# Optimization experiments

Hardware: AMD Instinct MI355X
Metric: run time of the kernel (lower is better)

## Reference

```python
import jax, jax.numpy as jnp
import numpy as np

N_HEADS = 32
N_KV_HEADS = 8
HEAD_DIM = 64
D_MODEL = 2048
SLIDING_WINDOW = 512
ROPE_THETA = 10000.0
PAST_LENGTH = 0
EPS = 1e-6


def setup_inputs() -> dict:
    key = jax.random.key(0)
    k1, k2, k3 = jax.random.split(key, 3)
    B, S = 1, 2048
    q_size = N_HEADS * HEAD_DIM
    kv_size = N_KV_HEADS * HEAD_DIM
    return {
        "x": jax.random.normal(k1, (B, S, D_MODEL), dtype=jnp.float32),
        "w_qkv": jax.random.normal(k2, (q_size + 2 * kv_size, D_MODEL), dtype=jnp.float32) * (D_MODEL ** -0.5),
        "w_out": jax.random.normal(k3, (D_MODEL, q_size), dtype=jnp.float32) * (q_size ** -0.5),
        "q_norm_w": jnp.ones((HEAD_DIM,), dtype=jnp.float32),
        "k_norm_w": jnp.ones((HEAD_DIM,), dtype=jnp.float32),
    }


def _rms_norm(x, w):
    xf = x.astype(jnp.float32)
    rms = jax.lax.rsqrt(jnp.mean(xf * xf, axis=-1, keepdims=True) + EPS)
    return (xf * rms).astype(x.dtype) * w


def _rope(q, k, past_length):
    # q: [b, h, s, d], k: [b, kv, s, d]
    s, d = q.shape[2], q.shape[3]
    inv_freq = 1.0 / (ROPE_THETA ** (jnp.arange(0, d, 2, dtype=jnp.float32) / d))
    pos = jnp.arange(s, dtype=jnp.float32) + past_length
    ang = pos[:, None] * inv_freq[None, :]            # [s, d/2]
    emb = jnp.concatenate([ang, ang], axis=-1)        # [s, d]
    cos, sin = jnp.cos(emb), jnp.sin(emb)

    def rot_half(x):
        x1, x2 = jnp.split(x, 2, axis=-1)
        return jnp.concatenate([-x2, x1], axis=-1)

    q = q * cos + rot_half(q) * sin
    k = k * cos + rot_half(k) * sin
    return q, k


def _sliding_mask(seq_len, total_len, past_length):
    q_idx = jnp.arange(seq_len)[:, None]
    k_idx = jnp.arange(total_len)[None, :]
    causal = (q_idx + past_length) >= k_idx
    window = (q_idx + past_length - k_idx) < SLIDING_WINDOW
    keep = causal & window
    return jnp.where(keep, 0.0, -jnp.inf).astype(jnp.float32)[None, None]


def reference(x, w_qkv, w_out, q_norm_w, k_norm_w):
    b, s, _ = x.shape
    n_rep = N_HEADS // N_KV_HEADS
    q_size = N_HEADS * HEAD_DIM
    kv_size = N_KV_HEADS * HEAD_DIM

    qkv = jnp.einsum('bsd,od->bso', x, w_qkv)
    q, k, v = jnp.split(qkv, [q_size, q_size + kv_size], axis=-1)
    q = q.reshape(b, s, N_HEADS, HEAD_DIM).transpose(0, 2, 1, 3)
    k = k.reshape(b, s, N_KV_HEADS, HEAD_DIM).transpose(0, 2, 1, 3)
    v = v.reshape(b, s, N_KV_HEADS, HEAD_DIM).transpose(0, 2, 1, 3)

    q = _rms_norm(q, q_norm_w)
    k = _rms_norm(k, k_norm_w)
    q, k = _rope(q, k, PAST_LENGTH)

    k_rep = jnp.repeat(k, n_rep, axis=1)  # [b, H, s, d]
    v_rep = jnp.repeat(v, n_rep, axis=1)

    scale = HEAD_DIM ** -0.5
    scores = jnp.einsum('bhqd,bhkd->bhqk', q, k_rep) * scale
    scores = scores + _sliding_mask(s, s, PAST_LENGTH)
    probs = jax.nn.softmax(scores, axis=-1)
    attn = jnp.einsum('bhqk,bhkd->bhqd', probs, v_rep)

    attn = attn.transpose(0, 2, 1, 3).reshape(b, s, q_size)
    return jnp.einsum('bso,do->bsd', attn, w_out)
```

## Files before the change

kernel.cpp:

```cpp
#include <hip/hip_runtime.h>

typedef unsigned short u16;
typedef unsigned int u32;
typedef __bf16 bf16x8 __attribute__((ext_vector_type(8)));
typedef float f32x4 __attribute__((ext_vector_type(4)));
typedef float f32x16 __attribute__((ext_vector_type(16)));
typedef u16 u16x8 __attribute__((ext_vector_type(8)));
typedef u32 u32x2 __attribute__((ext_vector_type(2)));
typedef u32 u32x4 __attribute__((ext_vector_type(4)));

#define MFMA16(a, b, c) __builtin_amdgcn_mfma_f32_16x16x32_bf16((a), (b), (c), 0, 0, 0)
#define MFMA32(a, b, c) __builtin_amdgcn_mfma_f32_32x32x16_bf16((a), (b), (c), 0, 0, 0)

__device__ __forceinline__ u16 f2bf(float f) {
    unsigned int u = __float_as_uint(f);
    u = (u + 0x7FFF + ((u >> 16) & 1)) >> 16;
    return (u16)u;
}

__device__ __forceinline__ u32 cvtpk(float a, float b) {
    u32 d;
    asm("v_cvt_pk_bf16_f32 %0, %1, %2" : "=v"(d) : "v"(a), "v"(b));
    return d;
}

__device__ __forceinline__ void gld_lds16(const u16* g, u16* l) {
    __builtin_amdgcn_global_load_lds(
        (const __attribute__((address_space(1))) unsigned int*)g,
        (__attribute__((address_space(3))) unsigned int*)l, 16, 0, 0);
}

__global__ __launch_bounds__(256) void cvt_bf16(const float* __restrict__ in,
                                                u16* __restrict__ out, int n4) {
    int idx = blockIdx.x * blockDim.x + threadIdx.x;
    int stride = gridDim.x * blockDim.x;
    for (int i = idx; i < n4; i += stride) {
        float4 v = reinterpret_cast<const float4*>(in)[i];
        ushort4 o;
        o.x = f2bf(v.x); o.y = f2bf(v.y); o.z = f2bf(v.z); o.w = f2bf(v.w);
        reinterpret_cast<ushort4*>(out)[i] = o;
    }
}

__global__ __launch_bounds__(256) void reduce_add(const float4* __restrict__ a,
                                                  const float4* __restrict__ b,
                                                  float4* __restrict__ o, int n4) {
    int idx = blockIdx.x * blockDim.x + threadIdx.x;
    int stride = gridDim.x * blockDim.x;
    for (int i = idx; i < n4; i += stride) {
        float4 va = a[i], vb = b[i];
        float4 vo = {va.x + vb.x, va.y + vb.y, va.z + vb.z, va.w + vb.w};
        o[i] = vo;
    }
}

template <int SPLITK>
__global__ __launch_bounds__(256) void gemm_bt(const u16* __restrict__ A,
                                               const u16* __restrict__ B,
                                               float* __restrict__ C,
                                               int M, int N, int K) {
    __shared__ __align__(16) u16 As[2][128 * 32];
    __shared__ __align__(16) u16 Bs[2][128 * 32];

    int nbn = N >> 7;
    int bid = blockIdx.x;
    int nwg = (M >> 7) * nbn;
    int cpx = nwg >> 3;
    int wg = (bid & 7) * cpx + (bid >> 3);
    int tm = wg / nbn, tn = wg % nbn;
    int m0 = tm << 7, n0 = tn << 7;

    int Ks = K / SPLITK;
    int kbase = blockIdx.y * Ks;
    float* Cs = C + (size_t)blockIdx.y * ((size_t)M * N);

    int t = threadIdx.x;
    int w = t >> 6, l = t & 63, lrow = l & 15, lhi = l >> 4;
    int wr = w >> 1, wc = w & 1;

    int e0 = t * 8;
    int row0 = e0 >> 5, col0 = e0 & 31;

    const u16* Ag = A + (size_t)m0 * K + kbase;
    const u16* Bg = B + (size_t)n0 * K + kbase;

    auto stage = [&](int sbuf, int kt) {
        int k0 = kt << 5;
        gld_lds16(Ag + (size_t)row0 * K + k0 + col0, &As[sbuf][e0]);
        gld_lds16(Ag + (size_t)(row0 + 64) * K + k0 + col0, &As[sbuf][e0 + 2048]);
        gld_lds16(Bg + (size_t)row0 * K + k0 + col0, &Bs[sbuf][e0]);
        gld_lds16(Bg + (size_t)(row0 + 64) * K + k0 + col0, &Bs[sbuf][e0 + 2048]);
    };

    f32x4 acc[4][4] = {};
    int NT = Ks >> 5;
    stage(0, 0);
    __syncthreads();
    int buf = 0;
    for (int kt = 0; kt < NT; ++kt) {
        if (kt + 1 < NT) stage(buf ^ 1, kt + 1);
        bf16x8 af[4], bfr[4];
#pragma unroll
        for (int i = 0; i < 4; ++i) {
            af[i]  = *(const bf16x8*)&As[buf][(wr * 64 + i * 16 + lrow) * 32 + lhi * 8];
            bfr[i] = *(const bf16x8*)&Bs[buf][(wc * 64 + i * 16 + lrow) * 32 + lhi * 8];
        }
#pragma unroll
        for (int i = 0; i < 4; ++i)
#pragma unroll
            for (int j = 0; j < 4; ++j)
                acc[i][j] = MFMA16(af[i], bfr[j], acc[i][j]);
        __syncthreads();
        buf ^= 1;
    }
#pragma unroll
    for (int i = 0; i < 4; ++i) {
#pragma unroll
        for (int j = 0; j < 4; ++j) {
            int crow = m0 + wr * 64 + i * 16 + lhi * 4;
            int ccol = n0 + wc * 64 + j * 16 + lrow;
            float* cp = Cs + (size_t)crow * N + ccol;
#pragma unroll
            for (int r2 = 0; r2 < 4; ++r2) cp[(size_t)r2 * N] = acc[i][j][r2];
        }
    }
}

__global__ __launch_bounds__(256) void qkv_post(const float* __restrict__ qkv0,
                                                const float* __restrict__ qkv1,
                                                const float* __restrict__ qw,
                                                const float* __restrict__ kw,
                                                u16* __restrict__ qb,
                                                u16* __restrict__ kb,
                                                u16* __restrict__ vb) {
    const float C = 0.18033688011112042f;
    int s = blockIdx.x;
    int t = threadIdx.x, w = t >> 6, lane = t & 63;
    const float* row0 = qkv0 + (size_t)s * 3072;
    const float* row1 = qkv1 + (size_t)s * 3072;
    int d2 = lane & 31;
    float inv = exp2f(-(float)d2 * (13.287712379549449f / 32.0f));
    float ang = (float)s * inv;
    float cs = cosf(ang), sn = sinf(ang);
    for (int h = w; h < 48; h += 4) {
        float v = row0[h * 64 + lane] + row1[h * 64 + lane];
        if (h < 40) {
            float ss = v * v;
#pragma unroll
            for (int m = 32; m; m >>= 1) ss += __shfl_xor(ss, m);
            float rms = rsqrtf(ss * (1.0f / 64.0f) + 1e-6f);
            float wgt = (h < 32) ? qw[lane] : kw[lane];
            v = v * rms * wgt;
            float part = __shfl_xor(v, 32);
            float rot = (lane < 32) ? -part : part;
            v = v * cs + rot * sn;
            if (h < 32)
                qb[((size_t)h * 2048 + s) * 64 + lane] = f2bf(v * C);
            else
                kb[((size_t)(h - 32) * 2048 + s) * 64 + lane] = f2bf(v);
        } else {
            vb[((size_t)(h - 40) * 2048 + s) * 64 + lane] = f2bf(v);
        }
    }
}

__global__ __launch_bounds__(256) void transpose_v(const u16* __restrict__ vb,
                                                   u16* __restrict__ vt) {
    int kv = blockIdx.y;
    int s0 = blockIdx.x * 256;
    __shared__ __align__(16) u16 tile[64][256];
    int t = threadIdx.x;
    int sl = t >> 3;
    int d0 = (t & 7) * 8;
#pragma unroll
    for (int j = 0; j < 8; ++j) {
        int s = sl + j * 32;
        u16x8 v = *(const u16x8*)(vb + ((size_t)kv * 2048 + s0 + s) * 64 + d0);
#pragma unroll
        for (int e = 0; e < 8; ++e) tile[d0 + e][s] = v[e];
    }
    __syncthreads();
    int d = t >> 2;
    int so = (t & 3) * 64;
#pragma unroll
    for (int j = 0; j < 8; ++j) {
        int s_local = so + j * 8;
        *(u16x8*)(vt + ((size_t)kv * 64 + d) * 2048 + s0 + s_local) =
            *(const u16x8*)&tile[d][s_local];
    }
}

__global__ __launch_bounds__(256) void attn_fa4(const u16* __restrict__ qb,
                                                const u16* __restrict__ kb,
                                                const u16* __restrict__ vt,
                                                u16* __restrict__ ab) {
    int h = blockIdx.y, kv = h >> 2;
    int t = threadIdx.x, w = t >> 6, l = t & 63;
    int lq = l & 31, hi = l >> 5;
    int qlo = blockIdx.x * 32;
    __shared__ float Olds[4][64][32];
    __shared__ float llds[4][32];

    const u16* qrow = qb + ((size_t)h * 2048 + qlo + lq) * 64 + hi * 8;
    bf16x8 qf[4];
#pragma unroll
    for (int dk = 0; dk < 4; ++dk) qf[dk] = *(const bf16x8*)(qrow + dk * 16);

    f32x16 oa = {}, ob = {};
    float lsum = 0.f;

    int kstart = qlo - 511; if (kstart < 0) kstart = 0;
    int kt0 = kstart >> 5, kt1 = qlo >> 5;
    const u16* kb_h = kb + (size_t)kv * 2048 * 64;
    const u16* vt_h = vt + (size_t)kv * 64 * 2048;

    for (int kt = kt0 + w; kt <= kt1; kt += 4) {
        int k0 = kt << 5;
        const u16* krow = kb_h + (size_t)(k0 + lq) * 64 + hi * 8;
        bf16x8 kf0 = *(const bf16x8*)(krow);
        bf16x8 kf1 = *(const bf16x8*)(krow + 16);
        bf16x8 kf2 = *(const bf16x8*)(krow + 32);
        bf16x8 kf3 = *(const bf16x8*)(krow + 48);
        const u16* vrow = vt_h + (size_t)lq * 2048 + k0 + hi * 8;
        bf16x8 va0 = *(const bf16x8*)(vrow);
        bf16x8 va1 = *(const bf16x8*)(vrow + 16);
        bf16x8 vb0 = *(const bf16x8*)(vrow + 32 * 2048);
        bf16x8 vb1 = *(const bf16x8*)(vrow + 32 * 2048 + 16);

        f32x16 s = {};
        s = MFMA32(kf0, qf[0], s);
        s = MFMA32(kf1, qf[1], s);
        s = MFMA32(kf2, qf[2], s);
        s = MFMA32(kf3, qf[3], s);

        bool edge = (k0 + 31 > qlo) || (qlo + 31 - k0 >= 512);
        if (edge) {
            int q = qlo + lq;
#pragma unroll
            for (int r = 0; r < 16; ++r) {
                int k = k0 + (r & 3) + 8 * (r >> 2) + 4 * hi;
                if (!((unsigned)(q - k) < 512u)) s[r] = -1e30f;
            }
        }
        float p[16];
#pragma unroll
        for (int r = 0; r < 16; ++r) {
            p[r] = exp2f(s[r]);
            lsum += p[r];
        }

        u32 pk0 = cvtpk(p[0], p[1]),   pk1 = cvtpk(p[2], p[3]);
        u32 pk2 = cvtpk(p[4], p[5]),   pk3 = cvtpk(p[6], p[7]);
        u32 pk4 = cvtpk(p[8], p[9]),   pk5 = cvtpk(p[10], p[11]);
        u32 pk6 = cvtpk(p[12], p[13]), pk7 = cvtpk(p[14], p[15]);
        u32x2 r02 = __builtin_amdgcn_permlane32_swap(pk0, pk2, false, false);
        u32x2 r13 = __builtin_amdgcn_permlane32_swap(pk1, pk3, false, false);
        u32x2 r46 = __builtin_amdgcn_permlane32_swap(pk4, pk6, false, false);
        u32x2 r57 = __builtin_amdgcn_permlane32_swap(pk5, pk7, false, false);
        bf16x8 b0, b1;
        {
            u32* bp = (u32*)&b0;
            bp[0] = r02[0]; bp[1] = r13[0]; bp[2] = r02[1]; bp[3] = r13[1];
            u32* bq = (u32*)&b1;
            bq[0] = r46[0]; bq[1] = r57[0]; bq[2] = r46[1]; bq[3] = r57[1];
        }
        oa = MFMA32(va0, b0, oa);
        oa = MFMA32(va1, b1, oa);
        ob = MFMA32(vb0, b0, ob);
        ob = MFMA32(vb1, b1, ob);
    }

    lsum += __shfl_xor(lsum, 32);
#pragma unroll
    for (int r = 0; r < 16; ++r) {
        int d = (r & 3) + 8 * (r >> 2) + 4 * hi;
        Olds[w][d][lq]      = oa[r];
        Olds[w][d + 32][lq] = ob[r];
    }
    if (hi == 0) llds[w][lq] = lsum;
    __syncthreads();

    int q = t & 31, dg = t >> 5;
    float lt = llds[0][q] + llds[1][q] + llds[2][q] + llds[3][q];
    float inv = 1.0f / lt;
    float v[8];
#pragma unroll
    for (int e = 0; e < 8; ++e) {
        int d = dg * 8 + e;
        v[e] = (Olds[0][d][q] + Olds[1][d][q] +
                Olds[2][d][q] + Olds[3][d][q]) * inv;
    }
    u32x4 pkt = { cvtpk(v[0], v[1]), cvtpk(v[2], v[3]),
                  cvtpk(v[4], v[5]), cvtpk(v[6], v[7]) };
    *(u32x4*)(ab + (size_t)(qlo + q) * 2048 + h * 64 + dg * 8) = pkt;
}

extern "C" void kernel_launch(void* const* d_in, const int* in_sizes, int n_in,
                              void* d_out, int out_size, void* d_ws, size_t ws_size,
                              hipStream_t stream) {
    const float* x     = (const float*)d_in[0];
    const float* w_qkv = (const float*)d_in[1];
    const float* w_out = (const float*)d_in[2];
    const float* qw    = (const float*)d_in[3];
    const float* kw    = (const float*)d_in[4];
    float* out = (float*)d_out;

    char* ws = (char*)d_ws;
    u16*   x_b    = (u16*)(ws);
    u16*   wB     = (u16*)(ws + 8388608);
    u16*   q_b    = (u16*)(ws);
    u16*   k_b    = (u16*)(ws + 8388608);
    u16*   v_b    = (u16*)(ws + 10485760);
    u16*   v_t    = (u16*)(ws + 12582912);
    float* P0     = (float*)(ws + 20971520);
    float* O0     = (float*)(ws + 20971520);
    float* O1     = (float*)(ws + 37748736);
    u16*   attn_b = (u16*)(ws + 54525952);

    cvt_bf16<<<2048, 256, 0, stream>>>(x, x_b, 2048 * 2048 / 4);
    cvt_bf16<<<2048, 256, 0, stream>>>(w_qkv, wB, 3072 * 2048 / 4);
    gemm_bt<2><<<dim3(384, 2), 256, 0, stream>>>(x_b, wB, P0, 2048, 3072, 2048);
    qkv_post<<<2048, 256, 0, stream>>>(P0, P0 + (size_t)2048 * 3072, qw, kw, q_b, k_b, v_b);
    transpose_v<<<dim3(8, 8), 256, 0, stream>>>(v_b, v_t);
    attn_fa4<<<dim3(64, 32), 256, 0, stream>>>(q_b, k_b, v_t, attn_b);
    cvt_bf16<<<2048, 256, 0, stream>>>(w_out, wB, 2048 * 2048 / 4);
    gemm_bt<2><<<dim3(256, 2), 256, 0, stream>>>(attn_b, wB, O0, 2048, 2048, 2048);
    reduce_add<<<1024, 256, 0, stream>>>((const float4*)O0, (const float4*)O1,
                                         (float4*)out, 2048 * 2048 / 4);
}
```

Measured before the change: 147.1 us.

## Use 8-wave GEMM tiles and software-prefetch K tiles in attention

The bf16 GEMM now launches 512 threads per block with a 2x4 wave grid. Each wave computes a 64x32 sub-tile, so staging needs one global-to-LDS load per thread per operand instead of two. This should raise occupancy and latency hiding at the cost of more B-fragment LDS reads per MFMA. The attention kernel double-buffers the K fragments in registers, loading the next tile's K while the current tile is computed, to overlap global-load latency with MFMA and softmax work; this costs extra registers.

```diff
diff --git a/kernel.cpp b/kernel.cpp
--- a/kernel.cpp
+++ b/kernel.cpp
@@ -55,7 +55,7 @@
 }
 
 template <int SPLITK>
-__global__ __launch_bounds__(256) void gemm_bt(const u16* __restrict__ A,
+__global__ __launch_bounds__(512) void gemm_bt(const u16* __restrict__ A,
                                                const u16* __restrict__ B,
                                                float* __restrict__ C,
                                                int M, int N, int K) {
@@ -76,7 +76,7 @@
 
     int t = threadIdx.x;
     int w = t >> 6, l = t & 63, lrow = l & 15, lhi = l >> 4;
-    int wr = w >> 1, wc = w & 1;
+    int wr = w >> 2, wc = w & 3;
 
     int e0 = t * 8;
     int row0 = e0 >> 5, col0 = e0 & 31;
@@ -87,28 +87,27 @@
     auto stage = [&](int sbuf, int kt) {
         int k0 = kt << 5;
         gld_lds16(Ag + (size_t)row0 * K + k0 + col0, &As[sbuf][e0]);
-        gld_lds16(Ag + (size_t)(row0 + 64) * K + k0 + col0, &As[sbuf][e0 + 2048]);
         gld_lds16(Bg + (size_t)row0 * K + k0 + col0, &Bs[sbuf][e0]);
-        gld_lds16(Bg + (size_t)(row0 + 64) * K + k0 + col0, &Bs[sbuf][e0 + 2048]);
     };
 
-    f32x4 acc[4][4] = {};
+    f32x4 acc[4][2] = {};
     int NT = Ks >> 5;
     stage(0, 0);
     __syncthreads();
     int buf = 0;
     for (int kt = 0; kt < NT; ++kt) {
         if (kt + 1 < NT) stage(buf ^ 1, kt + 1);
-        bf16x8 af[4], bfr[4];
-#pragma unroll
-        for (int i = 0; i < 4; ++i) {
-            af[i]  = *(const bf16x8*)&As[buf][(wr * 64 + i * 16 + lrow) * 32 + lhi * 8];
-            bfr[i] = *(const bf16x8*)&Bs[buf][(wc * 64 + i * 16 + lrow) * 32 + lhi * 8];
-        }
+        bf16x8 af[4], bfr[2];
 #pragma unroll
         for (int i = 0; i < 4; ++i)
-#pragma unroll
-            for (int j = 0; j < 4; ++j)
+            af[i] = *(const bf16x8*)&As[buf][(wr * 64 + i * 16 + lrow) * 32 + lhi * 8];
+#pragma unroll
+        for (int j = 0; j < 2; ++j)
+            bfr[j] = *(const bf16x8*)&Bs[buf][(wc * 32 + j * 16 + lrow) * 32 + lhi * 8];
+#pragma unroll
+        for (int i = 0; i < 4; ++i)
+#pragma unroll
+            for (int j = 0; j < 2; ++j)
                 acc[i][j] = MFMA16(af[i], bfr[j], acc[i][j]);
         __syncthreads();
         buf ^= 1;
@@ -116,9 +115,9 @@
 #pragma unroll
     for (int i = 0; i < 4; ++i) {
 #pragma unroll
-        for (int j = 0; j < 4; ++j) {
+        for (int j = 0; j < 2; ++j) {
             int crow = m0 + wr * 64 + i * 16 + lhi * 4;
-            int ccol = n0 + wc * 64 + j * 16 + lrow;
+            int ccol = n0 + wc * 32 + j * 16 + lrow;
             float* cp = Cs + (size_t)crow * N + ccol;
 #pragma unroll
             for (int r2 = 0; r2 < 4; ++r2) cp[(size_t)r2 * N] = acc[i][j][r2];
@@ -190,7 +189,7 @@
     }
 }
 
-__global__ __launch_bounds__(256) void attn_fa4(const u16* __restrict__ qb,
+__global__ __launch_bounds__(256) void attn_fa5(const u16* __restrict__ qb,
                                                 const u16* __restrict__ kb,
                                                 const u16* __restrict__ vt,
                                                 u16* __restrict__ ab) {
@@ -214,25 +213,22 @@
     const u16* kb_h = kb + (size_t)kv * 2048 * 64;
     const u16* vt_h = vt + (size_t)kv * 64 * 2048;
 
-    for (int kt = kt0 + w; kt <= kt1; kt += 4) {
-        int k0 = kt << 5;
-        const u16* krow = kb_h + (size_t)(k0 + lq) * 64 + hi * 8;
-        bf16x8 kf0 = *(const bf16x8*)(krow);
-        bf16x8 kf1 = *(const bf16x8*)(krow + 16);
-        bf16x8 kf2 = *(const bf16x8*)(krow + 32);
-        bf16x8 kf3 = *(const bf16x8*)(krow + 48);
-        const u16* vrow = vt_h + (size_t)lq * 2048 + k0 + hi * 8;
-        bf16x8 va0 = *(const bf16x8*)(vrow);
-        bf16x8 va1 = *(const bf16x8*)(vrow + 16);
-        bf16x8 vb0 = *(const bf16x8*)(vrow + 32 * 2048);
-        bf16x8 vb1 = *(const bf16x8*)(vrow + 32 * 2048 + 16);
-
+#define LOADK(k0_, f0, f1, f2, f3)                                          \
+    { const u16* kr_ = kb_h + (size_t)((k0_) + lq) * 64 + hi * 8;           \
+      f0 = *(const bf16x8*)(kr_);       f1 = *(const bf16x8*)(kr_ + 16);    \
+      f2 = *(const bf16x8*)(kr_ + 32);  f3 = *(const bf16x8*)(kr_ + 48); }
+#define LOADV(k0_, a0, a1, b0, b1)                                          \
+    { const u16* vr_ = vt_h + (size_t)lq * 2048 + (k0_) + hi * 8;           \
+      a0 = *(const bf16x8*)(vr_);              a1 = *(const bf16x8*)(vr_ + 16); \
+      b0 = *(const bf16x8*)(vr_ + 32 * 2048);  b1 = *(const bf16x8*)(vr_ + 32 * 2048 + 16); }
+
+    auto dotile = [&](int k0, bf16x8 kf0, bf16x8 kf1, bf16x8 kf2, bf16x8 kf3,
+                      bf16x8 va0, bf16x8 va1, bf16x8 vb0, bf16x8 vb1) {
         f32x16 s = {};
         s = MFMA32(kf0, qf[0], s);
         s = MFMA32(kf1, qf[1], s);
         s = MFMA32(kf2, qf[2], s);
         s = MFMA32(kf3, qf[3], s);
-
         bool edge = (k0 + 31 > qlo) || (qlo + 31 - k0 >= 512);
         if (edge) {
             int q = qlo + lq;
@@ -248,7 +244,6 @@
             p[r] = exp2f(s[r]);
             lsum += p[r];
         }
-
         u32 pk0 = cvtpk(p[0], p[1]),   pk1 = cvtpk(p[2], p[3]);
         u32 pk2 = cvtpk(p[4], p[5]),   pk3 = cvtpk(p[6], p[7]);
         u32 pk4 = cvtpk(p[8], p[9]),   pk5 = cvtpk(p[10], p[11]);
@@ -268,7 +263,25 @@
         oa = MFMA32(va1, b1, oa);
         ob = MFMA32(vb0, b0, ob);
         ob = MFMA32(vb1, b1, ob);
-    }
+    };
+
+    bf16x8 kA0, kA1, kA2, kA3, kB0, kB1, kB2, kB3;
+    bf16x8 va0, va1, vb0, vb1;
+    int kt = kt0 + w;
+    if (kt <= kt1) LOADK(kt << 5, kA0, kA1, kA2, kA3);
+    while (kt <= kt1) {
+        LOADV(kt << 5, va0, va1, vb0, vb1);
+        if (kt + 4 <= kt1) LOADK((kt + 4) << 5, kB0, kB1, kB2, kB3);
+        dotile(kt << 5, kA0, kA1, kA2, kA3, va0, va1, vb0, vb1);
+        kt += 4;
+        if (kt > kt1) break;
+        LOADV(kt << 5, va0, va1, vb0, vb1);
+        if (kt + 4 <= kt1) LOADK((kt + 4) << 5, kA0, kA1, kA2, kA3);
+        dotile(kt << 5, kB0, kB1, kB2, kB3, va0, va1, vb0, vb1);
+        kt += 4;
+    }
+#undef LOADK
+#undef LOADV
 
     lsum += __shfl_xor(lsum, 32);
 #pragma unroll
@@ -319,12 +332,12 @@
 
     cvt_bf16<<<2048, 256, 0, stream>>>(x, x_b, 2048 * 2048 / 4);
     cvt_bf16<<<2048, 256, 0, stream>>>(w_qkv, wB, 3072 * 2048 / 4);
-    gemm_bt<2><<<dim3(384, 2), 256, 0, stream>>>(x_b, wB, P0, 2048, 3072, 2048);
+    gemm_bt<2><<<dim3(384, 2), 512, 0, stream>>>(x_b, wB, P0, 2048, 3072, 2048);
     qkv_post<<<2048, 256, 0, stream>>>(P0, P0 + (size_t)2048 * 3072, qw, kw, q_b, k_b, v_b);
     transpose_v<<<dim3(8, 8), 256, 0, stream>>>(v_b, v_t);
-    attn_fa4<<<dim3(64, 32), 256, 0, stream>>>(q_b, k_b, v_t, attn_b);
+    attn_fa5<<<dim3(64, 32), 256, 0, stream>>>(q_b, k_b, v_t, attn_b);
     cvt_bf16<<<2048, 256, 0, stream>>>(w_out, wB, 2048 * 2048 / 4);
-    gemm_bt<2><<<dim3(256, 2), 256, 0, stream>>>(attn_b, wB, O0, 2048, 2048, 2048);
+    gemm_bt<2><<<dim3(256, 2), 512, 0, stream>>>(attn_b, wB, O0, 2048, 2048, 2048);
     reduce_add<<<1024, 256, 0, stream>>>((const float4*)O0, (const float4*)O1,
                                          (float4*)out, 2048 * 2048 / 4);
 }
```

Measured after the change: 154.6 us. 5.1% more time.
